# Performance work log

Hardware: AMD Instinct MI355X
Metric: run time of the kernel (lower is better)

## Reference

```python
import jax, jax.numpy as jnp
import numpy as np

NUM_CAPSULE = 16
DIM_CAPSULE = 64
ROUTINGS = 3
T_EPS = 1e-07


def squash(v, axis=-1):
    # NOTE: this repo's 'squash' is v / sqrt(||v||^2 + eps) (norm-only scaling)
    s = jnp.sum(v * v, axis=axis, keepdims=True)
    return v / jnp.sqrt(s + T_EPS)


def setup_inputs() -> dict:
    key = jax.random.key(0)
    k1, k2 = jax.random.split(key)
    B, N_in, D_in = 64, 512, 1024
    x = jax.random.normal(k1, (B, N_in, D_in), dtype=jnp.float32)
    # xavier-normal-ish init for W [1, D_in, num_capsule*dim_capsule]
    fan_in, fan_out = D_in, NUM_CAPSULE * DIM_CAPSULE
    std = float(np.sqrt(2.0 / (fan_in + fan_out)))
    W = jax.random.normal(k2, (1, D_in, NUM_CAPSULE * DIM_CAPSULE), dtype=jnp.float32) * std
    return {"x": x, "W": W}


def reference(x, W):
    B, N_in, D_in = x.shape
    # u_hat: [B, N_in, num_cap*dim_cap] -> [B, num_cap, N_in, dim_cap]
    u_hat = jnp.matmul(x, W[0])
    u_hat = u_hat.reshape(B, N_in, NUM_CAPSULE, DIM_CAPSULE).transpose(0, 2, 1, 3)
    b = jnp.zeros((B, NUM_CAPSULE, N_in), dtype=u_hat.dtype)
    outputs = None
    for i in range(ROUTINGS):
        # torch code permutes to [B, N_in, num_cap], softmaxes dim=2, permutes back:
        # equivalent to softmax over the num_capsule axis (axis=1)
        c = jax.nn.softmax(b, axis=1)  # [B, num_cap, N_in]
        outputs = squash(jnp.einsum('bij,bijk->bik', c, u_hat))  # [B, num_cap, dim_cap]
        if i < ROUTINGS - 1:
            b = jnp.einsum('bik,bijk->bij', outputs, u_hat)  # [B, num_cap, N_in]
    return outputs
```

## Files before the change

### kernel.cpp

```cpp
#include <hip/hip_runtime.h>
#include <stdint.h>

#define NUM_CAP 16
#define DIM_CAP 64
#define BATCH   64
#define N_IN    512
#define D_IN    1024
#define N_COL   1024
#define M_ROWS  (BATCH*N_IN)

typedef __attribute__((ext_vector_type(8))) short short8;
typedef __attribute__((ext_vector_type(4))) float f32x4;

__device__ __forceinline__ float bf2f(unsigned int u) {
  return __uint_as_float(u << 16);
}
__device__ __forceinline__ unsigned short f2bf_rne(float f) {
  unsigned int x = __float_as_uint(f);
  x += 0x7fffu + ((x >> 16) & 1u);
  return (unsigned short)(x >> 16);
}
__device__ __forceinline__ unsigned int pack_rne(unsigned int lo, unsigned int hi) {
  const unsigned int lr = lo + (0x7fffu + ((lo >> 16) & 1u));
  const unsigned int hr = hi + (0x7fffu + ((hi >> 16) & 1u));
  return (lr >> 16) | (hr & 0xffff0000u);
}

__global__ __launch_bounds__(256) void prep(
    const float* __restrict__ x, const float* __restrict__ W,
    unsigned short* __restrict__ xb, unsigned short* __restrict__ Wt) {
  const int t = threadIdx.x;
  if (blockIdx.x < 16384) {
    const size_t i = ((size_t)blockIdx.x * 256 + t) * 8;
    const uint4 a = *(const uint4*)(x + i);
    const uint4 b = *(const uint4*)(x + i + 4);
    uint4 p;
    p.x = pack_rne(a.x, a.y); p.y = pack_rne(a.z, a.w);
    p.z = pack_rne(b.x, b.y); p.w = pack_rne(b.z, b.w);
    *(uint4*)(xb + i) = p;
  } else {
    __shared__ float tile[32][33];
    const int bid = blockIdx.x - 16384;
    const int bx = bid & 31, by = bid >> 5;
    const int tx = t & 31, ty0 = t >> 5;
    #pragma unroll
    for (int r = 0; r < 4; r++) {
      const int ty = ty0 + r * 8;
      tile[ty][tx] = W[(size_t)(by * 32 + ty) * N_COL + bx * 32 + tx];
    }
    __syncthreads();
    #pragma unroll
    for (int r = 0; r < 4; r++) {
      const int ty = ty0 + r * 8;
      Wt[(size_t)(bx * 32 + ty) * D_IN + by * 32 + tx] = f2bf_rne(tile[tx][ty]);
    }
  }
}

__global__ __launch_bounds__(256) void gemm_uhat(
    const unsigned short* __restrict__ A,
    const unsigned short* __restrict__ Bt,
    unsigned short* __restrict__ C) {
  __shared__ __align__(16) unsigned short lA[128 * 32];
  __shared__ __align__(16) unsigned short lB[128 * 32];

  const int t = threadIdx.x;
  const int wave = t >> 6, lane = t & 63;
  const int xcd = blockIdx.x & 7, local = blockIdx.x >> 3;
  const int mt = xcd * 32 + (local >> 3), nt = local & 7;
  const int m0 = mt * 128, n0 = nt * 128;
  const int wm = wave & 1, wn = wave >> 1;

  f32x4 acc[4][4] = {};

  const int srow = lane >> 2;
  const int schunk = ((lane & 3) ^ ((srow >> 1) & 3)) * 8;

  for (int kt = 0; kt < D_IN / 32; ++kt) {
    const int k0 = kt * 32;
    __syncthreads();
    #pragma unroll
    for (int s0 = 0; s0 < 2; ++s0) {
      const int s = wave + s0 * 4;
      const unsigned short* ga = A + (size_t)(m0 + s * 16 + srow) * D_IN + k0 + schunk;
      __builtin_amdgcn_global_load_lds(
          (const __attribute__((address_space(1))) void*)ga,
          (__attribute__((address_space(3))) void*)(lA + s * 512), 16, 0, 0);
      const unsigned short* gb = Bt + (size_t)(n0 + s * 16 + srow) * D_IN + k0 + schunk;
      __builtin_amdgcn_global_load_lds(
          (const __attribute__((address_space(1))) void*)gb,
          (__attribute__((address_space(3))) void*)(lB + s * 512), 16, 0, 0);
    }
    __syncthreads();

    short8 af[4], bfr[4];
    const int rsel = lane & 15;
    const int q = lane >> 4;
    const int koff = (q ^ ((rsel >> 1) & 3)) * 8;
    #pragma unroll
    for (int tm = 0; tm < 4; tm++)
      af[tm] = *(const short8*)&lA[(wm * 64 + tm * 16 + rsel) * 32 + koff];
    #pragma unroll
    for (int tn = 0; tn < 4; tn++)
      bfr[tn] = *(const short8*)&lB[(wn * 64 + tn * 16 + rsel) * 32 + koff];
    #pragma unroll
    for (int tm = 0; tm < 4; tm++)
      #pragma unroll
      for (int tn = 0; tn < 4; tn++)
        acc[tm][tn] = __builtin_amdgcn_mfma_f32_16x16x32_bf16(
            af[tm], bfr[tn], acc[tm][tn], 0, 0, 0);
  }

  const int lrow = (lane >> 4) * 4, lcol = lane & 15;
  #pragma unroll
  for (int tm = 0; tm < 4; tm++)
    #pragma unroll
    for (int tn = 0; tn < 4; tn++)
      #pragma unroll
      for (int r = 0; r < 4; r++) {
        const int row = m0 + wm * 64 + tm * 16 + lrow + r;
        const int col = n0 + wn * 64 + tn * 16 + lcol;
        C[(size_t)row * N_COL + col] = f2bf_rne(acc[tm][tn][r]);
      }
}

__global__ __launch_bounds__(256) void s1q(
    const unsigned short* __restrict__ uhat, float* __restrict__ S1q) {
  const int t = threadIdx.x;
  const int b = blockIdx.x >> 3, s = blockIdx.x & 7;
  const unsigned short* up =
      uhat + (size_t)(b * N_IN + s * 64) * N_COL + t * 4;
  float4 a = make_float4(0.f, 0.f, 0.f, 0.f);
  #pragma unroll 8
  for (int j = 0; j < 64; ++j, up += N_COL) {
    const uint2 d = *(const uint2*)up;
    a.x += bf2f(d.x & 0xffffu);
    a.y += __uint_as_float(d.x & 0xffff0000u);
    a.z += bf2f(d.y & 0xffffu);
    a.w += __uint_as_float(d.y & 0xffff0000u);
  }
  *(float4*)&S1q[(size_t)blockIdx.x * 1024 + t * 4] = a;
}

__global__ __launch_bounds__(256) void route_mid(
    const unsigned short* __restrict__ uhat,
    const float* __restrict__ Vin,
    float* __restrict__ Pout,
    const int nstrips) {
  __shared__ float sq[16 * 68];
  __shared__ float red[4][1024];
  const int t = threadIdx.x;
  const int w = t >> 6, lane = t & 63;
  const int b = blockIdx.x >> 4, jt4 = blockIdx.x & 15;
  const int jt = jt4 * 4 + w;
  const int i_l = lane >> 2, c4 = lane & 3;

  float4 v4 = make_float4(0.f, 0.f, 0.f, 0.f);
  for (int s = 0; s < nstrips; ++s) {
    const float4 ps = *(const float4*)&Vin[((size_t)b * nstrips + s) * 1024 + t * 4];
    v4.x += ps.x; v4.y += ps.y; v4.z += ps.z; v4.w += ps.w;
  }
  float ss = v4.x * v4.x + v4.y * v4.y + v4.z * v4.z + v4.w * v4.w;
  #pragma unroll
  for (int d = 1; d < 16; d <<= 1) ss += __shfl_xor(ss, d);
  const float inv = 1.f / sqrtf(ss + 1e-7f);
  const int oi = t >> 4, ok = (t & 15) * 4;
  *(float4*)&sq[oi * 68 + ok] =
      make_float4(v4.x * inv, v4.y * inv, v4.z * inv, v4.w * inv);
  __syncthreads();

  float pv[16];
  #pragma unroll
  for (int q = 0; q < 4; q++)
    *(float4*)&pv[q * 4] = *(const float4*)&sq[i_l * 68 + c4 * 16 + q * 4];

  float acc[16];
  #pragma unroll
  for (int q = 0; q < 16; q++) acc[q] = 0.f;

  const unsigned short* ub =
      uhat + (size_t)(b * N_IN + jt * 8) * N_COL + lane * 16;

  for (int jj = 0; jj < 8; ++jj, ub += N_COL) {
    const uint4 d0 = *(const uint4*)ub;
    const uint4 d1 = *(const uint4*)(ub + 8);
    float u[16];
    #define UNP(wd, o) { u[(o)] = bf2f((wd) & 0xffffu); u[(o)+1] = __uint_as_float((wd) & 0xffff0000u); }
    UNP(d0.x, 0) UNP(d0.y, 2) UNP(d0.z, 4) UNP(d0.w, 6)
    UNP(d1.x, 8) UNP(d1.y, 10) UNP(d1.z, 12) UNP(d1.w, 14)
    #undef UNP

    float dot = 0.f;
    #pragma unroll
    for (int q = 0; q < 16; q++) dot = fmaf(pv[q], u[q], dot);
    dot += __shfl_xor(dot, 1);
    dot += __shfl_xor(dot, 2);
    const float e = __expf(dot);
    float s = e;
    #pragma unroll
    for (int d = 4; d < 64; d <<= 1) s += __shfl_xor(s, d);
    const float c = e / s;
    #pragma unroll
    for (int q = 0; q < 16; q++) acc[q] = fmaf(c, u[q], acc[q]);
  }

  #pragma unroll
  for (int q = 0; q < 4; q++)
    *(float4*)&red[w][lane * 16 + q * 4] = make_float4(
        acc[q * 4 + 0], acc[q * 4 + 1], acc[q * 4 + 2], acc[q * 4 + 3]);
  __syncthreads();
  float4 s4 = make_float4(0.f, 0.f, 0.f, 0.f);
  #pragma unroll
  for (int ww = 0; ww < 4; ++ww) {
    const float4 r = *(const float4*)&red[ww][t * 4];
    s4.x += r.x; s4.y += r.y; s4.z += r.z; s4.w += r.w;
  }
  *(float4*)&Pout[(size_t)blockIdx.x * 1024 + t * 4] = s4;
}

__global__ __launch_bounds__(64) void route_last(
    const float* __restrict__ P, float* __restrict__ dst) {
  const int bi = blockIdx.x;
  const int k = threadIdx.x;
  const int b = bi >> 4, i = bi & 15;
  const float* p = P + (size_t)b * 16 * 1024 + i * 64 + k;
  float s = 0.f;
  #pragma unroll
  for (int tt = 0; tt < 16; ++tt) s += p[(size_t)tt * 1024];
  float ss = s * s;
  #pragma unroll
  for (int d = 1; d < 64; d <<= 1) ss += __shfl_xor(ss, d);
  dst[bi * 64 + k] = s / sqrtf(ss + 1e-7f);
}

extern "C" void kernel_launch(void* const* d_in, const int* in_sizes, int n_in,
                              void* d_out, int out_size, void* d_ws, size_t ws_size,
                              hipStream_t stream) {
  const float* x = (const float*)d_in[0];
  const float* W = (const float*)d_in[1];
  float* out = (float*)d_out;

  char* ws = (char*)d_ws;
  unsigned short* Wt   = (unsigned short*)ws;
  unsigned short* uhat = (unsigned short*)(ws + (size_t)(2 << 20));
  unsigned short* xb   = (unsigned short*)(ws + (size_t)66 * (1 << 20));
  float* S1 = (float*)(ws + (size_t)130 * (1 << 20));
  float* P1 = (float*)(ws + (size_t)66 * (1 << 20));
  float* P2 = (float*)(ws + (size_t)71 * (1 << 20));

  prep<<<16384 + 1024, 256, 0, stream>>>(x, W, xb, Wt);
  gemm_uhat<<<2048, 256, 0, stream>>>(xb, Wt, uhat);
  s1q<<<512, 256, 0, stream>>>(uhat, S1);
  route_mid<<<1024, 256, 0, stream>>>(uhat, S1, P1, 8);
  route_mid<<<1024, 256, 0, stream>>>(uhat, P1, P2, 16);
  route_last<<<1024, 64, 0, stream>>>(P2, out);
}
```

Before: 321.2 us.

## Rewrite u_hat GEMM as 256x256 tile, 8-wave, double-buffered pipelined kernel

The bf16 GEMM that produces u_hat moves from 128x128 tiles with 4 waves and a single LDS buffer to 256x256 tiles with 8 waves. Each K-step is 64 wide and the 128 KB of LDS is double-buffered. Global-to-LDS loads for the next stage are interleaved across eight quadrant phases, with explicit vmcnt waits, barriers and setprio around the MFMA bursts, so loads overlap compute and data is reused more per tile. The risks are lower occupancy from the large LDS footprint and more registers, fewer blocks (512), and hand-tuned wait counts that must be exactly right.

```diff
diff --git a/kernel.cpp b/kernel.cpp
--- a/kernel.cpp
+++ b/kernel.cpp
@@ -57,71 +57,121 @@
   }
 }
 
-__global__ __launch_bounds__(256) void gemm_uhat(
+#define LA_OFF(d, h, ks) (((d)*2 + (h))*2 + (ks)) * 4096
+#define LB_OFF(d, h, ks) (32768 + ((((d)*2 + (h))*2 + (ks)) * 4096))
+
+__global__ __launch_bounds__(512) void gemm_uhat(
     const unsigned short* __restrict__ A,
     const unsigned short* __restrict__ Bt,
     unsigned short* __restrict__ C) {
-  __shared__ __align__(16) unsigned short lA[128 * 32];
-  __shared__ __align__(16) unsigned short lB[128 * 32];
+  __shared__ __align__(16) unsigned short lds[65536];
 
   const int t = threadIdx.x;
   const int wave = t >> 6, lane = t & 63;
+  const int wm = wave >> 2, wn = wave & 3;
+
   const int xcd = blockIdx.x & 7, local = blockIdx.x >> 3;
-  const int mt = xcd * 32 + (local >> 3), nt = local & 7;
-  const int m0 = mt * 128, n0 = nt * 128;
-  const int wm = wave & 1, wn = wave >> 1;
-
-  f32x4 acc[4][4] = {};
-
-  const int srow = lane >> 2;
-  const int schunk = ((lane & 3) ^ ((srow >> 1) & 3)) * 8;
-
-  for (int kt = 0; kt < D_IN / 32; ++kt) {
-    const int k0 = kt * 32;
-    __syncthreads();
-    #pragma unroll
-    for (int s0 = 0; s0 < 2; ++s0) {
-      const int s = wave + s0 * 4;
-      const unsigned short* ga = A + (size_t)(m0 + s * 16 + srow) * D_IN + k0 + schunk;
-      __builtin_amdgcn_global_load_lds(
-          (const __attribute__((address_space(1))) void*)ga,
-          (__attribute__((address_space(3))) void*)(lA + s * 512), 16, 0, 0);
-      const unsigned short* gb = Bt + (size_t)(n0 + s * 16 + srow) * D_IN + k0 + schunk;
-      __builtin_amdgcn_global_load_lds(
-          (const __attribute__((address_space(1))) void*)gb,
-          (__attribute__((address_space(3))) void*)(lB + s * 512), 16, 0, 0);
-    }
-    __syncthreads();
-
-    short8 af[4], bfr[4];
-    const int rsel = lane & 15;
-    const int q = lane >> 4;
-    const int koff = (q ^ ((rsel >> 1) & 3)) * 8;
-    #pragma unroll
-    for (int tm = 0; tm < 4; tm++)
-      af[tm] = *(const short8*)&lA[(wm * 64 + tm * 16 + rsel) * 32 + koff];
-    #pragma unroll
-    for (int tn = 0; tn < 4; tn++)
-      bfr[tn] = *(const short8*)&lB[(wn * 64 + tn * 16 + rsel) * 32 + koff];
-    #pragma unroll
-    for (int tm = 0; tm < 4; tm++)
+  const int mt = xcd * 16 + (local >> 2), nt = local & 3;
+  const int m0 = mt * 256, n0 = nt * 256;
+
+  const int srl = t >> 2;
+  const int scz = (t & 3) ^ ((t >> 3) & 3);
+  const unsigned short* aBase = A  + (size_t)(m0 + srl) * D_IN + scz * 8;
+  const unsigned short* bBase = Bt + (size_t)(n0 + srl) * D_IN + scz * 8;
+
+#define STG_A(kt, h) do { \
+    _Pragma("unroll") \
+    for (int c_ = 0; c_ < 2; ++c_) \
+      __builtin_amdgcn_global_load_lds( \
+        (const __attribute__((address_space(1))) void*)(aBase + (size_t)(h)*128*D_IN + (kt)*64 + c_*32), \
+        (__attribute__((address_space(3))) void*)(lds + (LA_OFF(((kt)&1), (h), c_)) + t*8), \
+        16, 0, 0); \
+  } while (0)
+#define STG_B(kt, h) do { \
+    _Pragma("unroll") \
+    for (int c_ = 0; c_ < 2; ++c_) \
+      __builtin_amdgcn_global_load_lds( \
+        (const __attribute__((address_space(1))) void*)(bBase + (size_t)(h)*128*D_IN + (kt)*64 + c_*32), \
+        (__attribute__((address_space(3))) void*)(lds + (LB_OFF(((kt)&1), (h), c_)) + t*8), \
+        16, 0, 0); \
+  } while (0)
+
+  f32x4 acc[2][2][4][2] = {};
+
+  const int rsel = lane & 15;
+  const int koff = ((lane >> 4) ^ ((rsel >> 1) & 3)) * 8;
+
+#define PHASE(d_, qm_, qn_, STAGES, WAITS) do { \
+    short8 af[4][2], bfr[2][2]; \
+    _Pragma("unroll") \
+    for (int mf = 0; mf < 4; ++mf) \
+      _Pragma("unroll") \
+      for (int ks = 0; ks < 2; ++ks) \
+        af[mf][ks] = *(const short8*)&lds[(LA_OFF((d_), (qm_), ks)) + (wm*64 + mf*16 + rsel)*32 + koff]; \
+    _Pragma("unroll") \
+    for (int nf = 0; nf < 2; ++nf) \
+      _Pragma("unroll") \
+      for (int ks = 0; ks < 2; ++ks) \
+        bfr[nf][ks] = *(const short8*)&lds[(LB_OFF((d_), (qn_), ks)) + (wn*32 + nf*16 + rsel)*32 + koff]; \
+    STAGES; \
+    __builtin_amdgcn_s_barrier(); \
+    __builtin_amdgcn_s_setprio(1); \
+    _Pragma("unroll") \
+    for (int ks = 0; ks < 2; ++ks) \
+      _Pragma("unroll") \
+      for (int mf = 0; mf < 4; ++mf) \
+        _Pragma("unroll") \
+        for (int nf = 0; nf < 2; ++nf) \
+          acc[qm_][qn_][mf][nf] = __builtin_amdgcn_mfma_f32_16x16x32_bf16( \
+              af[mf][ks], bfr[nf][ks], acc[qm_][qn_][mf][nf], 0, 0, 0); \
+    __builtin_amdgcn_s_setprio(0); \
+    asm volatile("s_waitcnt lgkmcnt(0)" ::: "memory"); \
+    __builtin_amdgcn_sched_barrier(0); \
+    WAITS; \
+    __builtin_amdgcn_s_barrier(); \
+  } while (0)
+
+#define VMC(n) asm volatile("s_waitcnt vmcnt(" #n ")" ::: "memory")
+
+  STG_A(0, 0); STG_B(0, 0); STG_B(0, 1); STG_A(0, 1);
+  STG_A(1, 0); STG_B(1, 1);
+  VMC(6);
+  __builtin_amdgcn_s_barrier();
+
+  for (int i = 0; i < 8; ++i) {
+    const int u = 2 * i, v = 2 * i + 1;
+    const bool st = (i < 7);
+    PHASE(0, 0, 0, { STG_B(v, 0); }, {});
+    PHASE(0, 0, 1, { STG_A(v, 1); }, { VMC(8); });
+    PHASE(0, 1, 1, { if (st) STG_A(u + 2, 0); }, {});
+    PHASE(0, 1, 0, { if (st) STG_B(u + 2, 1); },
+          { if (st) { VMC(6); } else { VMC(2); } });
+    PHASE(1, 0, 0, { if (st) STG_B(u + 2, 0); }, {});
+    PHASE(1, 0, 1, { if (st) STG_A(u + 2, 1); },
+          { if (st) { VMC(8); } else { VMC(0); } });
+    PHASE(1, 1, 1, { if (st) STG_A(v + 2, 0); }, {});
+    PHASE(1, 1, 0, { if (st) STG_B(v + 2, 1); }, { VMC(6); });
+  }
+
+  const int lrow = (lane >> 4) * 4, lcol = lane & 15;
+  #pragma unroll
+  for (int qm = 0; qm < 2; ++qm)
+    #pragma unroll
+    for (int qn = 0; qn < 2; ++qn)
       #pragma unroll
-      for (int tn = 0; tn < 4; tn++)
-        acc[tm][tn] = __builtin_amdgcn_mfma_f32_16x16x32_bf16(
-            af[tm], bfr[tn], acc[tm][tn], 0, 0, 0);
-  }
-
-  const int lrow = (lane >> 4) * 4, lcol = lane & 15;
-  #pragma unroll
-  for (int tm = 0; tm < 4; tm++)
-    #pragma unroll
-    for (int tn = 0; tn < 4; tn++)
-      #pragma unroll
-      for (int r = 0; r < 4; r++) {
-        const int row = m0 + wm * 64 + tm * 16 + lrow + r;
-        const int col = n0 + wn * 64 + tn * 16 + lcol;
-        C[(size_t)row * N_COL + col] = f2bf_rne(acc[tm][tn][r]);
-      }
+      for (int mf = 0; mf < 4; ++mf)
+        #pragma unroll
+        for (int nf = 0; nf < 2; ++nf)
+          #pragma unroll
+          for (int r = 0; r < 4; ++r) {
+            const int row = m0 + qm * 128 + wm * 64 + mf * 16 + lrow + r;
+            const int col = n0 + qn * 128 + wn * 32 + nf * 16 + lcol;
+            C[(size_t)row * N_COL + col] = f2bf_rne(acc[qm][qn][mf][nf][r]);
+          }
+#undef PHASE
+#undef VMC
+#undef STG_A
+#undef STG_B
 }
 
 __global__ __launch_bounds__(256) void s1q(
@@ -249,7 +299,7 @@
   float* P2 = (float*)(ws + (size_t)71 * (1 << 20));
 
   prep<<<16384 + 1024, 256, 0, stream>>>(x, W, xb, Wt);
-  gemm_uhat<<<2048, 256, 0, stream>>>(xb, Wt, uhat);
+  gemm_uhat<<<512, 512, 0, stream>>>(xb, Wt, uhat);
   s1q<<<512, 256, 0, stream>>>(uhat, S1);
   route_mid<<<1024, 256, 0, stream>>>(uhat, S1, P1, 8);
   route_mid<<<1024, 256, 0, stream>>>(uhat, P1, P2, 16);
```

Result: faster. 312.8 us (-2.6%).

## Reassociate routing through W to avoid materializing u_hat

Applied to the files above, without the earlier changes.

Replaces the full x·W GEMM that materialized u_hat with an algebraically reassociated routing. First-iteration outputs come from column sums of x times W. Agreement logits are computed as x·(W·v), and weighted sums as (c^T x)·W, all in fp32 CUDA-core code. This removes the bf16 GEMM and the repeated reads of the 64MB u_hat, but x (128MB fp32) is now streamed three times. Several small GEMV kernels run with only 64 blocks, which leaves the GPU underfilled.

```diff
diff --git a/kernel.cpp b/kernel.cpp
--- a/kernel.cpp
+++ b/kernel.cpp
@@ -6,231 +6,156 @@
 #define BATCH   64
 #define N_IN    512
 #define D_IN    1024
-#define N_COL   1024
-#define M_ROWS  (BATCH*N_IN)
 
-typedef __attribute__((ext_vector_type(8))) short short8;
-typedef __attribute__((ext_vector_type(4))) float f32x4;
 
-__device__ __forceinline__ float bf2f(unsigned int u) {
-  return __uint_as_float(u << 16);
-}
-__device__ __forceinline__ unsigned short f2bf_rne(float f) {
-  unsigned int x = __float_as_uint(f);
-  x += 0x7fffu + ((x >> 16) & 1u);
-  return (unsigned short)(x >> 16);
-}
-__device__ __forceinline__ unsigned int pack_rne(unsigned int lo, unsigned int hi) {
-  const unsigned int lr = lo + (0x7fffu + ((lo >> 16) & 1u));
-  const unsigned int hr = hi + (0x7fffu + ((hi >> 16) & 1u));
-  return (lr >> 16) | (hr & 0xffff0000u);
+__global__ __launch_bounds__(256) void colsum8(
+    const float* __restrict__ x, float* __restrict__ cs8) {
+  const int t = threadIdx.x;
+  const int bid = blockIdx.x;
+  const float* p = x + (size_t)bid * 64 * 1024 + t * 4;
+  float4 a = make_float4(0.f, 0.f, 0.f, 0.f);
+  #pragma unroll 8
+  for (int j = 0; j < 64; ++j, p += 1024) {
+    const float4 d = *(const float4*)p;
+    a.x += d.x; a.y += d.y; a.z += d.z; a.w += d.w;
+  }
+  *(float4*)&cs8[(size_t)bid * 1024 + t * 4] = a;
 }
 
-__global__ __launch_bounds__(256) void prep(
-    const float* __restrict__ x, const float* __restrict__ W,
-    unsigned short* __restrict__ xb, unsigned short* __restrict__ Wt) {
+__global__ __launch_bounds__(256) void v_first(
+    const float* __restrict__ cs8, const float* __restrict__ W,
+    float* __restrict__ v) {
+  __shared__ float cs[1024];
+  const int t = threadIdx.x, b = blockIdx.x;
+  float4 a = make_float4(0.f, 0.f, 0.f, 0.f);
+  #pragma unroll
+  for (int s = 0; s < 8; ++s) {
+    const float4 d = *(const float4*)&cs8[(size_t)(b * 8 + s) * 1024 + t * 4];
+    a.x += d.x; a.y += d.y; a.z += d.z; a.w += d.w;
+  }
+  *(float4*)&cs[t * 4] = a;
+  __syncthreads();
+
+  float4 o = make_float4(0.f, 0.f, 0.f, 0.f);
+  #pragma unroll 8
+  for (int d = 0; d < 1024; ++d) {
+    const float c = cs[d];
+    const float4 w = *(const float4*)&W[(size_t)d * 1024 + t * 4];
+    o.x += c * w.x; o.y += c * w.y; o.z += c * w.z; o.w += c * w.w;
+  }
+  float ss = o.x * o.x + o.y * o.y + o.z * o.z + o.w * o.w;
+  #pragma unroll
+  for (int dd = 1; dd < 16; dd <<= 1) ss += __shfl_xor(ss, dd);
+  const float inv = 1.f / sqrtf(ss + 1e-7f);
+  *(float4*)&v[(size_t)b * 1024 + t * 4] =
+      make_float4(o.x * inv, o.y * inv, o.z * inv, o.w * inv);
+}
+
+__global__ __launch_bounds__(256) void wtilde(
+    const float* __restrict__ v, const float* __restrict__ W,
+    float* __restrict__ wt) {
+  __shared__ float vl[1024];
   const int t = threadIdx.x;
-  if (blockIdx.x < 16384) {
-    const size_t i = ((size_t)blockIdx.x * 256 + t) * 8;
-    const uint4 a = *(const uint4*)(x + i);
-    const uint4 b = *(const uint4*)(x + i + 4);
-    uint4 p;
-    p.x = pack_rne(a.x, a.y); p.y = pack_rne(a.z, a.w);
-    p.z = pack_rne(b.x, b.y); p.w = pack_rne(b.z, b.w);
-    *(uint4*)(xb + i) = p;
-  } else {
-    __shared__ float tile[32][33];
-    const int bid = blockIdx.x - 16384;
-    const int bx = bid & 31, by = bid >> 5;
-    const int tx = t & 31, ty0 = t >> 5;
+  const int b = blockIdx.x >> 4, dblk = blockIdx.x & 15;
+  *(float4*)&vl[t * 4] = *(const float4*)&v[(size_t)b * 1024 + t * 4];
+  __syncthreads();
+  const int d = dblk * 64 + (t >> 2), q = t & 3;
+  const float* wrow = W + (size_t)d * 1024 + q * 256;
+  #pragma unroll
+  for (int ii = 0; ii < 4; ++ii) {
+    const int i = q * 4 + ii;
+    float dot = 0.f;
     #pragma unroll
-    for (int r = 0; r < 4; r++) {
-      const int ty = ty0 + r * 8;
-      tile[ty][tx] = W[(size_t)(by * 32 + ty) * N_COL + bx * 32 + tx];
+    for (int m = 0; m < 16; ++m) {
+      const float4 w = *(const float4*)&wrow[ii * 64 + m * 4];
+      dot += w.x * vl[i * 64 + m * 4]     + w.y * vl[i * 64 + m * 4 + 1]
+           + w.z * vl[i * 64 + m * 4 + 2] + w.w * vl[i * 64 + m * 4 + 3];
     }
-    __syncthreads();
-    #pragma unroll
-    for (int r = 0; r < 4; r++) {
-      const int ty = ty0 + r * 8;
-      Wt[(size_t)(bx * 32 + ty) * D_IN + by * 32 + tx] = f2bf_rne(tile[tx][ty]);
-    }
+    wt[((size_t)b * 16 + i) * 1024 + d] = dot;
   }
 }
 
-__global__ __launch_bounds__(256) void gemm_uhat(
-    const unsigned short* __restrict__ A,
-    const unsigned short* __restrict__ Bt,
-    unsigned short* __restrict__ C) {
-  __shared__ __align__(16) unsigned short lA[128 * 32];
-  __shared__ __align__(16) unsigned short lB[128 * 32];
+__global__ __launch_bounds__(256, 2) void bsoft_s(
+    const float* __restrict__ x, const float* __restrict__ wt,
+    float* __restrict__ sp) {
+  __shared__ float cv[2][16];
+  const int t = threadIdx.x;
+  const int b = blockIdx.x >> 3, jc = blockIdx.x & 7;
+  const int i = t >> 4, dr = t & 15;
 
-  const int t = threadIdx.x;
-  const int wave = t >> 6, lane = t & 63;
-  const int xcd = blockIdx.x & 7, local = blockIdx.x >> 3;
-  const int mt = xcd * 32 + (local >> 3), nt = local & 7;
-  const int m0 = mt * 128, n0 = nt * 128;
-  const int wm = wave & 1, wn = wave >> 1;
+  float4 wtr[16];
+  {
+    const float* wp = wt + ((size_t)b * 16 + i) * 1024 + dr * 64;
+    #pragma unroll
+    for (int m = 0; m < 16; ++m) wtr[m] = *(const float4*)&wp[m * 4];
+  }
+  float4 sac[16];
+  #pragma unroll
+  for (int m = 0; m < 16; ++m) sac[m] = make_float4(0.f, 0.f, 0.f, 0.f);
 
-  f32x4 acc[4][4] = {};
-
-  const int srow = lane >> 2;
-  const int schunk = ((lane & 3) ^ ((srow >> 1) & 3)) * 8;
-
-  for (int kt = 0; kt < D_IN / 32; ++kt) {
-    const int k0 = kt * 32;
+  const float* xp = x + (size_t)(b * 512 + jc * 64) * 1024 + dr * 64;
+  for (int j = 0; j < 64; ++j, xp += 1024) {
+    float4 xv[16];
+    #pragma unroll
+    for (int m = 0; m < 16; ++m) xv[m] = *(const float4*)&xp[m * 4];
+    float dot = 0.f;
+    #pragma unroll
+    for (int m = 0; m < 16; ++m)
+      dot += wtr[m].x * xv[m].x + wtr[m].y * xv[m].y
+           + wtr[m].z * xv[m].z + wtr[m].w * xv[m].w;
+    dot += __shfl_xor(dot, 1);
+    dot += __shfl_xor(dot, 2);
+    dot += __shfl_xor(dot, 4);
+    dot += __shfl_xor(dot, 8);
+    const float e = __expf(dot);
+    if (dr == 0) cv[j & 1][i] = e;
     __syncthreads();
+    float sum = 0.f;
     #pragma unroll
-    for (int s0 = 0; s0 < 2; ++s0) {
-      const int s = wave + s0 * 4;
-      const unsigned short* ga = A + (size_t)(m0 + s * 16 + srow) * D_IN + k0 + schunk;
-      __builtin_amdgcn_global_load_lds(
-          (const __attribute__((address_space(1))) void*)ga,
-          (__attribute__((address_space(3))) void*)(lA + s * 512), 16, 0, 0);
-      const unsigned short* gb = Bt + (size_t)(n0 + s * 16 + srow) * D_IN + k0 + schunk;
-      __builtin_amdgcn_global_load_lds(
-          (const __attribute__((address_space(1))) void*)gb,
-          (__attribute__((address_space(3))) void*)(lB + s * 512), 16, 0, 0);
+    for (int ii = 0; ii < 16; ++ii) sum += cv[j & 1][ii];
+    const float c = e / sum;
+    #pragma unroll
+    for (int m = 0; m < 16; ++m) {
+      sac[m].x += c * xv[m].x; sac[m].y += c * xv[m].y;
+      sac[m].z += c * xv[m].z; sac[m].w += c * xv[m].w;
     }
-    __syncthreads();
-
-    short8 af[4], bfr[4];
-    const int rsel = lane & 15;
-    const int q = lane >> 4;
-    const int koff = (q ^ ((rsel >> 1) & 3)) * 8;
-    #pragma unroll
-    for (int tm = 0; tm < 4; tm++)
-      af[tm] = *(const short8*)&lA[(wm * 64 + tm * 16 + rsel) * 32 + koff];
-    #pragma unroll
-    for (int tn = 0; tn < 4; tn++)
-      bfr[tn] = *(const short8*)&lB[(wn * 64 + tn * 16 + rsel) * 32 + koff];
-    #pragma unroll
-    for (int tm = 0; tm < 4; tm++)
-      #pragma unroll
-      for (int tn = 0; tn < 4; tn++)
-        acc[tm][tn] = __builtin_amdgcn_mfma_f32_16x16x32_bf16(
-            af[tm], bfr[tn], acc[tm][tn], 0, 0, 0);
   }
-
-  const int lrow = (lane >> 4) * 4, lcol = lane & 15;
+  float* spp = sp + ((size_t)blockIdx.x * 16 + i) * 1024 + dr * 64;
   #pragma unroll
-  for (int tm = 0; tm < 4; tm++)
-    #pragma unroll
-    for (int tn = 0; tn < 4; tn++)
-      #pragma unroll
-      for (int r = 0; r < 4; r++) {
-        const int row = m0 + wm * 64 + tm * 16 + lrow + r;
-        const int col = n0 + wn * 64 + tn * 16 + lcol;
-        C[(size_t)row * N_COL + col] = f2bf_rne(acc[tm][tn][r]);
-      }
+  for (int m = 0; m < 16; ++m) *(float4*)&spp[m * 4] = sac[m];
 }
 
-__global__ __launch_bounds__(256) void s1q(
-    const unsigned short* __restrict__ uhat, float* __restrict__ S1q) {
-  const int t = threadIdx.x;
-  const int b = blockIdx.x >> 3, s = blockIdx.x & 7;
-  const unsigned short* up =
-      uhat + (size_t)(b * N_IN + s * 64) * N_COL + t * 4;
-  float4 a = make_float4(0.f, 0.f, 0.f, 0.f);
-  #pragma unroll 8
-  for (int j = 0; j < 64; ++j, up += N_COL) {
-    const uint2 d = *(const uint2*)up;
-    a.x += bf2f(d.x & 0xffffu);
-    a.y += __uint_as_float(d.x & 0xffff0000u);
-    a.z += bf2f(d.y & 0xffffu);
-    a.w += __uint_as_float(d.y & 0xffff0000u);
+__global__ __launch_bounds__(256) void red_gemv_squash(
+    const float* __restrict__ sp, const float* __restrict__ W,
+    float* __restrict__ vout) {
+  __shared__ float sl[16 * 1028];
+  const int t = threadIdx.x, b = blockIdx.x;
+  for (int r = 0; r < 16; ++r) {
+    const int idx = r * 1024 + t * 4;
+    float4 a = make_float4(0.f, 0.f, 0.f, 0.f);
+    #pragma unroll
+    for (int p = 0; p < 8; ++p) {
+      const float4 d = *(const float4*)&sp[(size_t)(b * 8 + p) * 16384 + idx];
+      a.x += d.x; a.y += d.y; a.z += d.z; a.w += d.w;
+    }
+    *(float4*)&sl[r * 1028 + t * 4] = a;
   }
-  *(float4*)&S1q[(size_t)blockIdx.x * 1024 + t * 4] = a;
-}
-
-__global__ __launch_bounds__(256) void route_mid(
-    const unsigned short* __restrict__ uhat,
-    const float* __restrict__ Vin,
-    float* __restrict__ Pout,
-    const int nstrips) {
-  __shared__ float sq[16 * 68];
-  __shared__ float red[4][1024];
-  const int t = threadIdx.x;
-  const int w = t >> 6, lane = t & 63;
-  const int b = blockIdx.x >> 4, jt4 = blockIdx.x & 15;
-  const int jt = jt4 * 4 + w;
-  const int i_l = lane >> 2, c4 = lane & 3;
-
-  float4 v4 = make_float4(0.f, 0.f, 0.f, 0.f);
-  for (int s = 0; s < nstrips; ++s) {
-    const float4 ps = *(const float4*)&Vin[((size_t)b * nstrips + s) * 1024 + t * 4];
-    v4.x += ps.x; v4.y += ps.y; v4.z += ps.z; v4.w += ps.w;
-  }
-  float ss = v4.x * v4.x + v4.y * v4.y + v4.z * v4.z + v4.w * v4.w;
-  #pragma unroll
-  for (int d = 1; d < 16; d <<= 1) ss += __shfl_xor(ss, d);
-  const float inv = 1.f / sqrtf(ss + 1e-7f);
-  const int oi = t >> 4, ok = (t & 15) * 4;
-  *(float4*)&sq[oi * 68 + ok] =
-      make_float4(v4.x * inv, v4.y * inv, v4.z * inv, v4.w * inv);
   __syncthreads();
 
-  float pv[16];
+  const int i = t >> 4, kq = t & 15;
+  float4 o = make_float4(0.f, 0.f, 0.f, 0.f);
+  #pragma unroll 8
+  for (int d = 0; d < 1024; ++d) {
+    const float s = sl[i * 1028 + d];
+    const float4 w = *(const float4*)&W[(size_t)d * 1024 + i * 64 + kq * 4];
+    o.x += s * w.x; o.y += s * w.y; o.z += s * w.z; o.w += s * w.w;
+  }
+  float ss = o.x * o.x + o.y * o.y + o.z * o.z + o.w * o.w;
   #pragma unroll
-  for (int q = 0; q < 4; q++)
-    *(float4*)&pv[q * 4] = *(const float4*)&sq[i_l * 68 + c4 * 16 + q * 4];
-
-  float acc[16];
-  #pragma unroll
-  for (int q = 0; q < 16; q++) acc[q] = 0.f;
-
-  const unsigned short* ub =
-      uhat + (size_t)(b * N_IN + jt * 8) * N_COL + lane * 16;
-
-  for (int jj = 0; jj < 8; ++jj, ub += N_COL) {
-    const uint4 d0 = *(const uint4*)ub;
-    const uint4 d1 = *(const uint4*)(ub + 8);
-    float u[16];
-    #define UNP(wd, o) { u[(o)] = bf2f((wd) & 0xffffu); u[(o)+1] = __uint_as_float((wd) & 0xffff0000u); }
-    UNP(d0.x, 0) UNP(d0.y, 2) UNP(d0.z, 4) UNP(d0.w, 6)
-    UNP(d1.x, 8) UNP(d1.y, 10) UNP(d1.z, 12) UNP(d1.w, 14)
-    #undef UNP
-
-    float dot = 0.f;
-    #pragma unroll
-    for (int q = 0; q < 16; q++) dot = fmaf(pv[q], u[q], dot);
-    dot += __shfl_xor(dot, 1);
-    dot += __shfl_xor(dot, 2);
-    const float e = __expf(dot);
-    float s = e;
-    #pragma unroll
-    for (int d = 4; d < 64; d <<= 1) s += __shfl_xor(s, d);
-    const float c = e / s;
-    #pragma unroll
-    for (int q = 0; q < 16; q++) acc[q] = fmaf(c, u[q], acc[q]);
-  }
-
-  #pragma unroll
-  for (int q = 0; q < 4; q++)
-    *(float4*)&red[w][lane * 16 + q * 4] = make_float4(
-        acc[q * 4 + 0], acc[q * 4 + 1], acc[q * 4 + 2], acc[q * 4 + 3]);
-  __syncthreads();
-  float4 s4 = make_float4(0.f, 0.f, 0.f, 0.f);
-  #pragma unroll
-  for (int ww = 0; ww < 4; ++ww) {
-    const float4 r = *(const float4*)&red[ww][t * 4];
-    s4.x += r.x; s4.y += r.y; s4.z += r.z; s4.w += r.w;
-  }
-  *(float4*)&Pout[(size_t)blockIdx.x * 1024 + t * 4] = s4;
-}
-
-__global__ __launch_bounds__(64) void route_last(
-    const float* __restrict__ P, float* __restrict__ dst) {
-  const int bi = blockIdx.x;
-  const int k = threadIdx.x;
-  const int b = bi >> 4, i = bi & 15;
-  const float* p = P + (size_t)b * 16 * 1024 + i * 64 + k;
-  float s = 0.f;
-  #pragma unroll
-  for (int tt = 0; tt < 16; ++tt) s += p[(size_t)tt * 1024];
-  float ss = s * s;
-  #pragma unroll
-  for (int d = 1; d < 64; d <<= 1) ss += __shfl_xor(ss, d);
-  dst[bi * 64 + k] = s / sqrtf(ss + 1e-7f);
+  for (int dd = 1; dd < 16; dd <<= 1) ss += __shfl_xor(ss, dd);
+  const float inv = 1.f / sqrtf(ss + 1e-7f);
+  *(float4*)&vout[(size_t)b * 1024 + t * 4] =
+      make_float4(o.x * inv, o.y * inv, o.z * inv, o.w * inv);
 }
 
 extern "C" void kernel_launch(void* const* d_in, const int* in_sizes, int n_in,
@@ -241,17 +166,17 @@
   float* out = (float*)d_out;
 
   char* ws = (char*)d_ws;
-  unsigned short* Wt   = (unsigned short*)ws;
-  unsigned short* uhat = (unsigned short*)(ws + (size_t)(2 << 20));
-  unsigned short* xb   = (unsigned short*)(ws + (size_t)66 * (1 << 20));
-  float* S1 = (float*)(ws + (size_t)130 * (1 << 20));
-  float* P1 = (float*)(ws + (size_t)66 * (1 << 20));
-  float* P2 = (float*)(ws + (size_t)71 * (1 << 20));
+  float* cs8 = (float*)ws;
+  float* v   = (float*)(ws + (size_t)(2 << 20));
+  float* wt  = (float*)(ws + (size_t)(4 << 20));
+  float* sp  = (float*)(ws + (size_t)(8 << 20));
 
-  prep<<<16384 + 1024, 256, 0, stream>>>(x, W, xb, Wt);
-  gemm_uhat<<<2048, 256, 0, stream>>>(xb, Wt, uhat);
-  s1q<<<512, 256, 0, stream>>>(uhat, S1);
-  route_mid<<<1024, 256, 0, stream>>>(uhat, S1, P1, 8);
-  route_mid<<<1024, 256, 0, stream>>>(uhat, P1, P2, 16);
-  route_last<<<1024, 64, 0, stream>>>(P2, out);
+  colsum8<<<512, 256, 0, stream>>>(x, cs8);
+  v_first<<<64, 256, 0, stream>>>(cs8, W, v);
+  wtilde<<<1024, 256, 0, stream>>>(v, W, wt);
+  bsoft_s<<<512, 256, 0, stream>>>(x, wt, sp);
+  red_gemv_squash<<<64, 256, 0, stream>>>(sp, W, v);
+  wtilde<<<1024, 256, 0, stream>>>(v, W, wt);
+  bsoft_s<<<512, 256, 0, stream>>>(x, wt, sp);
+  red_gemv_squash<<<64, 256, 0, stream>>>(sp, W, out);
 }
```

New measurement: 919.9 us. +186.4%, slower.
